# Kernel optimization log

Hardware: AMD Instinct MI355X
Metric: run time of the kernel (lower is better)

Reference implementation:

```python
import jax, jax.numpy as jnp
import numpy as np

H = 128      # hidden_channels
L = 4        # num_layers
B = 8192     # graphs per batch
NB, NJ, NF = 4 * B, 12 * B, 4 * B   # base/joint/foot node counts (4 bases, 12 joints, 4 feet per graph)
NET = 8      # number of edge types


def _edges(key, E, n_src, n_dst):
    k1, k2 = jax.random.split(key)
    return jnp.stack([jax.random.randint(k1, (E,), 0, n_src),
                      jax.random.randint(k2, (E,), 0, n_dst)]).astype(jnp.int32)


def setup_inputs() -> dict:
    key = jax.random.key(0)
    ks = jax.random.split(key, 24)
    s = 0.02
    return {
        "x_base": jax.random.normal(ks[0], (NB, 1800), jnp.float32),
        "x_joint": jax.random.normal(ks[1], (NJ, 300), jnp.float32),
        "x_foot": jax.random.normal(ks[2], (NF, 900), jnp.float32),
        "enc_W_base": jax.random.normal(ks[3], (H, 1800), jnp.float32) * s,
        "enc_b_base": jnp.zeros((H,), jnp.float32),
        "enc_W_joint": jax.random.normal(ks[4], (H, 300), jnp.float32) * s,
        "enc_b_joint": jnp.zeros((H,), jnp.float32),
        "enc_W_foot": jax.random.normal(ks[5], (H, 900), jnp.float32) * s,
        "enc_b_foot": jnp.zeros((H,), jnp.float32),
        "conv_Wrel": jax.random.normal(ks[6], (L, NET, H, H), jnp.float32) * s,
        "conv_Wroot": jax.random.normal(ks[7], (L, NET, H, H), jnp.float32) * s,
        "conv_brel": jnp.zeros((L, NET, H), jnp.float32),
        "bt_W1": jax.random.normal(ks[8], (H, H), jnp.float32) * s,
        "bt_b1": jnp.zeros((H,), jnp.float32),
        "bt_W2": jax.random.normal(ks[9], (H, H), jnp.float32) * s,
        "bt_b2": jnp.zeros((H,), jnp.float32),
        "dec_W": jax.random.normal(ks[10], (24, 4 * H), jnp.float32) * s,
        "dec_b": jnp.zeros((24,), jnp.float32),
        "coeff_lin": jnp.ones((12,), jnp.float32),   # base_coefficients for linear dims (ones when symmetry_mode=None)
        "coeff_ang": jnp.ones((12,), jnp.float32),
        "ei_bb_gt": _edges(ks[11], NB, NB, NB),
        "ei_bb_gs": _edges(ks[12], NB, NB, NB),
        "ei_bb_gr": _edges(ks[13], NB, NB, NB),
        "ei_bj": _edges(ks[14], NB, NB, NJ),
        "ei_jb": _edges(ks[15], NB, NJ, NB),
        "ei_jj": _edges(ks[16], 4 * NB, NJ, NJ),
        "ei_jf": _edges(ks[17], NF, NJ, NF),
        "ei_fj": _edges(ks[18], NF, NF, NJ),
    }


def _forward(floats, eidx):
    (x_base, x_joint, x_foot, enc_W_base, enc_b_base, enc_W_joint, enc_b_joint,
     enc_W_foot, enc_b_foot, conv_Wrel, conv_Wroot, conv_brel,
     bt_W1, bt_b1, bt_W2, bt_b2, dec_W, dec_b, coeff_lin, coeff_ang) = floats
    ei_bb_gt, ei_bb_gs, ei_bb_gr, ei_bj, ei_jb, ei_jj, ei_jf, ei_fj = eidx
    N = {"base": x_base.shape[0], "joint": x_joint.shape[0], "foot": x_foot.shape[0]}
    # HeteroDictLinear encoder + activation
    x = {"base": jax.nn.relu(x_base @ enc_W_base.T + enc_b_base),
         "joint": jax.nn.relu(x_joint @ enc_W_joint.T + enc_b_joint),
         "foot": jax.nn.relu(x_foot @ enc_W_foot.T + enc_b_foot)}
    # (src_type, dst_type, edge_index, mean_aggr?) -- 'gt'/'gs' use mean, all others add
    etypes = [("base", "base", ei_bb_gt, True), ("base", "base", ei_bb_gs, True),
              ("base", "base", ei_bb_gr, False), ("base", "joint", ei_bj, False),
              ("joint", "base", ei_jb, False), ("joint", "joint", ei_jj, False),
              ("joint", "foot", ei_jf, False), ("foot", "joint", ei_fj, False)]
    for l in range(L):
        new = {k: jnp.zeros_like(v) for k, v in x.items()}
        for t, (s_t, d_t, ei, is_mean) in enumerate(etypes):
            msg = x[s_t][ei[0]]                                        # gather [E, H]
            agg = jax.ops.segment_sum(msg, ei[1], num_segments=N[d_t])  # scatter-add [N_dst, H]
            if is_mean:
                deg = jax.ops.segment_sum(jnp.ones((ei.shape[1],), msg.dtype), ei[1], num_segments=N[d_t])
                agg = agg / jnp.maximum(deg, 1.0)[:, None]
            # PyG GraphConv: lin_rel(aggr(x_src)) + lin_root(x_dst); HeteroConv aggr='sum' over edge types
            new[d_t] = new[d_t] + agg @ conv_Wrel[l, t].T + conv_brel[l, t] + x[d_t] @ conv_Wroot[l, t].T
        base_new = jax.nn.relu(new["base"] @ bt_W1.T + bt_b1) @ bt_W2.T + bt_b2
        x = {"base": base_new + x["base"],
             "joint": jax.nn.relu(new["joint"]) + x["joint"],
             "foot": jax.nn.relu(new["foot"]) + x["foot"]}
    bs = N["base"] // 4
    out = x["base"].reshape(bs, 4 * H) @ dec_W.T + dec_b             # [bs, 24]
    # morphological_symmetry_decoder (coeffs are ones when symmetry_mode=None)
    xr = out.reshape(bs, 4, 6)
    x_lin = (xr[:, :, :3].reshape(bs, 12) * coeff_lin).reshape(bs, 4, 3)
    x_ang = (xr[:, :, 3:].reshape(bs, 12) * coeff_ang).reshape(bs, 4, 3)
    return jnp.concatenate([x_lin, x_ang], axis=-1).reshape(bs, 24)


def reference(x_base, x_joint, x_foot, enc_W_base, enc_b_base, enc_W_joint, enc_b_joint,
              enc_W_foot, enc_b_foot, conv_Wrel, conv_Wroot, conv_brel,
              bt_W1, bt_b1, bt_W2, bt_b2, dec_W, dec_b, coeff_lin, coeff_ang,
              ei_bb_gt, ei_bb_gs, ei_bb_gr, ei_bj, ei_jb, ei_jj, ei_jf, ei_fj):
    floats = (x_base, x_joint, x_foot, enc_W_base, enc_b_base, enc_W_joint, enc_b_joint,
              enc_W_foot, enc_b_foot, conv_Wrel, conv_Wroot, conv_brel,
              bt_W1, bt_b1, bt_W2, bt_b2, dec_W, dec_b, coeff_lin, coeff_ang)
    eidx = (ei_bb_gt, ei_bb_gs, ei_bb_gr, ei_bj, ei_jb, ei_jj, ei_jf, ei_fj)
    return _forward(floats, eidx)
```

## Files before the change

### kernel.cpp

```cpp
#include <hip/hip_runtime.h>

typedef __bf16 bf16;
typedef __attribute__((ext_vector_type(8))) __bf16 bf16x8;
typedef __attribute__((ext_vector_type(4))) float f32x4;
typedef __attribute__((ext_vector_type(4))) int   i32x4;

#define NBASE  32768
#define NJOINT 98304
#define NFOOT  32768
#define NSLOT  458752
#define NEDGE  360448
#define SCAN_BLOCKS 448

static __device__ __forceinline__ f32x4 mfma16(bf16x8 a, bf16x8 b, f32x4 c) {
  return __builtin_amdgcn_mfma_f32_16x16x32_bf16(a, b, c, 0, 0, 0);
}

static __device__ __forceinline__ void edge_decomp(int slot, int& ty, int& e) {
  if (slot < 131072)      { ty = slot >> 15; e = slot & 32767; }
  else if (slot < 163840) { ty = 4; e = slot - 131072; }
  else if (slot < 294912) { ty = 5; e = slot - 163840; }
  else if (slot < 327680) { ty = 6; e = slot - 294912; }
  else                    { ty = 7; e = slot - 327680; }
}
static __device__ __forceinline__ int type_off(int ty) {
  return ty==0?0: ty==1?32768: ty==2?65536: ty==3?98304:
         ty==4?196608: ty==5?229376: ty==6?327680: 360448;
}

struct EArgs { const int* e0; const int* e1; const int* e2; const int* e3;
               const int* e4; const int* e5; const int* e6; const int* e7; };
static __device__ __forceinline__ const int* esel(const EArgs& a, int ty) {
  const int* p = a.e0;
  if (ty==1) p=a.e1; if (ty==2) p=a.e2; if (ty==3) p=a.e3;
  if (ty==4) p=a.e4; if (ty==5) p=a.e5; if (ty==6) p=a.e6; if (ty==7) p=a.e7;
  return p;
}

__global__ __launch_bounds__(256) void prep_kernel(
    const float* __restrict__ Wrel, const float* __restrict__ Wroot,
    const float* __restrict__ brel, const float* __restrict__ bt1,
    const float* __restrict__ bt2,
    bf16* __restrict__ Wrel_b, bf16* __restrict__ Wroot_b,
    float* __restrict__ bias_s, bf16* __restrict__ bt1_b, bf16* __restrict__ bt2_b)
{
  int t = blockIdx.x * 256 + threadIdx.x;
  if (t < 4*8*16384) Wrel_b[t] = (bf16)Wrel[t];
  if (t < 4*3*16384) {
    int i = t & 16383; int ld = t >> 14; int l = ld / 3, dt = ld - l*3;
    const float* Wb = Wroot + l * 8 * 16384;
    float s;
    if (dt == 0)      s = Wb[0*16384+i] + Wb[1*16384+i] + Wb[2*16384+i] + Wb[4*16384+i];
    else if (dt == 1) s = Wb[3*16384+i] + Wb[5*16384+i] + Wb[7*16384+i];
    else              s = Wb[6*16384+i];
    Wroot_b[t] = (bf16)s;
  }
  if (t < 16384) { bt1_b[t] = (bf16)bt1[t]; bt2_b[t] = (bf16)bt2[t]; }
  if (t < 4*3*128) {
    int c = t & 127; int ld = t >> 7; int l = ld / 3, dt = ld - l*3;
    const float* B = brel + l * 8 * 128;
    float s;
    if (dt == 0)      s = B[0*128+c] + B[1*128+c] + B[2*128+c] + B[4*128+c];
    else if (dt == 1) s = B[3*128+c] + B[5*128+c] + B[7*128+c];
    else              s = B[6*128+c];
    bias_s[t] = s;
  }
}

__global__ __launch_bounds__(256) void zero_kernel(int* cnt) {
  cnt[blockIdx.x * 256 + threadIdx.x] = 0;
}

__global__ __launch_bounds__(256) void hist8_kernel(EArgs a, int* __restrict__ cnt) {
  int slot = blockIdx.x * 256 + threadIdx.x;
  int ty, e; edge_decomp(slot, ty, e);
  const int* ep = esel(a, ty);
  int ecnt = (ty == 5) ? 131072 : 32768;
  int dst = ep[ecnt + e];
  atomicAdd(&cnt[type_off(ty) + dst], 1);
}

__global__ __launch_bounds__(256) void scanA_kernel(const int* __restrict__ cnt, int* __restrict__ bsum) {
  __shared__ int red[256];
  int base = blockIdx.x * 1024 + threadIdx.x * 4;
  i32x4 v = *(const i32x4*)(cnt + base);
  red[threadIdx.x] = v[0] + v[1] + v[2] + v[3];
  __syncthreads();
  for (int d = 128; d > 0; d >>= 1) {
    if (threadIdx.x < d) red[threadIdx.x] += red[threadIdx.x + d];
    __syncthreads();
  }
  if (threadIdx.x == 0) bsum[blockIdx.x] = red[0];
}

__global__ __launch_bounds__(256) void scanB_kernel(const int* __restrict__ bsum, int* __restrict__ bscan) {
  __shared__ int s[SCAN_BLOCKS];
  int i0 = threadIdx.x, i1 = threadIdx.x + 256;
  bool h1 = (i1 < SCAN_BLOCKS);
  s[i0] = bsum[i0];
  if (h1) s[i1] = bsum[i1];
  __syncthreads();
  for (int d = 1; d < SCAN_BLOCKS; d <<= 1) {
    int v0 = 0, v1 = 0;
    if (i0 >= d) v0 = s[i0 - d];
    if (h1 && i1 >= d) v1 = s[i1 - d];
    __syncthreads();
    s[i0] += v0;
    if (h1) s[i1] += v1;
    __syncthreads();
  }
  bscan[i0] = i0 ? s[i0 - 1] : 0;
  if (h1) bscan[i1] = s[i1 - 1];
}

__global__ __launch_bounds__(256) void scanC_kernel(const int* __restrict__ cnt,
    const int* __restrict__ bscan, int* __restrict__ rowptr, int* __restrict__ cursor)
{
  __shared__ int toff[256];
  int base = blockIdx.x * 1024 + threadIdx.x * 4;
  i32x4 v = *(const i32x4*)(cnt + base);
  int tsum = v[0] + v[1] + v[2] + v[3];
  toff[threadIdx.x] = tsum;
  __syncthreads();
  for (int d = 1; d < 256; d <<= 1) {
    int t = 0;
    if (threadIdx.x >= d) t = toff[threadIdx.x - d];
    __syncthreads();
    toff[threadIdx.x] += t;
    __syncthreads();
  }
  int off = bscan[blockIdx.x] + toff[threadIdx.x] - tsum;
  i32x4 r;
  r[0] = off; r[1] = off + v[0]; r[2] = off + v[0] + v[1]; r[3] = off + v[0] + v[1] + v[2];
  *(i32x4*)(rowptr + base) = r;
  *(i32x4*)(cursor + base) = r;
  if (blockIdx.x == SCAN_BLOCKS - 1 && threadIdx.x == 255) rowptr[NSLOT] = NEDGE;
}

__global__ __launch_bounds__(256) void fill_kernel(EArgs a, int* __restrict__ cursor,
                                                   int* __restrict__ perm) {
  int slot = blockIdx.x * 256 + threadIdx.x;
  int ty, e; edge_decomp(slot, ty, e);
  const int* ep = esel(a, ty);
  int ecnt = (ty == 5) ? 131072 : 32768;
  int src = ep[e];
  int dst = ep[ecnt + e];
  int pos = atomicAdd(&cursor[type_off(ty) + dst], 1);
  perm[pos] = src;
}

template<int K>
__global__ __launch_bounds__(256) void enc_kernel(
    const float* __restrict__ X, const float* __restrict__ W,
    const float* __restrict__ bvec, bf16* __restrict__ out, float* __restrict__ out32)
{
  __shared__ bf16 Wl[4*128*8];
  const int tid = threadIdx.x;
  const int lane = tid & 63, wv = tid >> 6;
  const int r = lane & 15, g = lane >> 4;
  const long row = (long)blockIdx.x * 64 + wv * 16 + r;
  f32x4 acc[8] = {};
  for (int kc = 0; kc < K; kc += 32) {
    __syncthreads();
    for (int i = tid; i < 512; i += 256) {
      int q = i & 3, n = i >> 2;
      int k0 = kc + 8*q;
      f32x4 a = {}; f32x4 b2 = {};
      if (k0 < K)     a  = *(const f32x4*)(W + (long)n*K + k0);
      if (k0 + 4 < K) b2 = *(const f32x4*)(W + (long)n*K + k0 + 4);
      bf16x8 pk;
      #pragma unroll
      for (int j = 0; j < 4; j++) { pk[j] = (bf16)a[j]; pk[4+j] = (bf16)b2[j]; }
      *(bf16x8*)&Wl[(q*128 + (n ^ q)) * 8] = pk;
    }
    __syncthreads();
    int k0 = kc + 8*g;
    f32x4 a0 = {}, a1 = {};
    if (k0 < K)     a0 = *(const f32x4*)(X + row*K + k0);
    if (k0 + 4 < K) a1 = *(const f32x4*)(X + row*K + k0 + 4);
    bf16x8 af;
    #pragma unroll
    for (int j = 0; j < 4; j++) { af[j] = (bf16)a0[j]; af[4+j] = (bf16)a1[j]; }
    const bf16* bp = &Wl[(g*128 + (r ^ g)) * 8];
    #pragma unroll
    for (int c = 0; c < 8; c++) {
      bf16x8 bfr = *(const bf16x8*)(bp + c*128);
      acc[c] = mfma16(af, bfr, acc[c]);
    }
  }
  const long rb = (long)blockIdx.x * 64 + wv * 16 + 4 * g;
  #pragma unroll
  for (int c = 0; c < 8; c++) {
    int col = 16*c + r;
    float bb = bvec[col];
    #pragma unroll
    for (int j = 0; j < 4; j++) {
      float v = acc[c][j] + bb;
      v = v > 0.f ? v : 0.f;
      out[(rb + j)*128 + col] = (bf16)v;
      out32[(rb + j)*128 + col] = v;
    }
  }
}

struct GDesc { const void* A; const bf16* W; const float* bias; const float* res32;
               void* out; void* out2; int nblk; };
struct GArgs { GDesc d[8]; };

template<int EPI, bool AF32, int NDESC>
__global__ __launch_bounds__(256) void gemm128_kernel(GArgs a)
{
  __shared__ bf16 Wl[16*128*8];
  int b = blockIdx.x, di = 0;
  while (di + 1 < NDESC && b >= a.d[di].nblk) { b -= a.d[di].nblk; ++di; }
  const GDesc& D = a.d[di];
  const int tid = threadIdx.x;
  const int lane = tid & 63, wv = tid >> 6;
  const int r = lane & 15, g = lane >> 4;
  for (int i = tid; i < 2048; i += 256) {
    int q = i & 15, n = i >> 4;
    bf16x8 v = *(const bf16x8*)(D.W + n*128 + q*8);
    *(bf16x8*)&Wl[(q*128 + (n ^ (q & 7))) * 8] = v;
  }
  const long row = (long)b * 64 + wv * 16 + r;
  bf16x8 af[4];
  if constexpr (AF32) {
    const float* A = (const float*)D.A;
    #pragma unroll
    for (int kk = 0; kk < 4; kk++) {
      f32x4 a0 = *(const f32x4*)(A + row*128 + kk*32 + 8*g);
      f32x4 a1 = *(const f32x4*)(A + row*128 + kk*32 + 8*g + 4);
      #pragma unroll
      for (int j = 0; j < 4; j++) { af[kk][j] = (bf16)a0[j]; af[kk][4+j] = (bf16)a1[j]; }
    }
  } else {
    const bf16* A = (const bf16*)D.A;
    #pragma unroll
    for (int kk = 0; kk < 4; kk++)
      af[kk] = *(const bf16x8*)(A + row*128 + kk*32 + 8*g);
  }
  __syncthreads();
  f32x4 acc[8] = {};
  #pragma unroll
  for (int kk = 0; kk < 4; kk++) {
    int q = kk*4 + g;
    const bf16* bp = &Wl[(q*128 + (r ^ (q & 7))) * 8];
    #pragma unroll
    for (int c = 0; c < 8; c++) {
      bf16x8 bfr = *(const bf16x8*)(bp + c*128);
      acc[c] = mfma16(af[kk], bfr, acc[c]);
    }
  }
  const long rb = (long)b * 64 + wv * 16 + 4 * g;
  #pragma unroll
  for (int c = 0; c < 8; c++) {
    int col = 16*c + r;
    #pragma unroll
    for (int j = 0; j < 4; j++) {
      float v = acc[c][j];
      long oidx = (rb + j)*128 + col;
      if constexpr (EPI == 0) {
        ((float*)D.out)[oidx] = v + D.bias[col];
      } else if constexpr (EPI == 1) {
        ((bf16*)D.out)[oidx] = (bf16)v;
      } else if constexpr (EPI == 2) {
        v += D.bias[col];
        v = v > 0.f ? v : 0.f;
        ((bf16*)D.out)[oidx] = (bf16)v;
      } else {
        v += D.bias[col] + D.res32[oidx];
        ((bf16*)D.out)[oidx] = (bf16)v;
        ((float*)D.out2)[oidx] = v;
      }
    }
  }
}

struct AArgs { const bf16* y[4]; const float* root; float* o32; bf16* o16; };

template<int KIND>
__global__ __launch_bounds__(256) void agg_kernel(AArgs a,
    const int* __restrict__ rowptr, const int* __restrict__ perm)
{
  constexpr int NT = (KIND==0) ? 4 : ((KIND==1) ? 3 : 1);
  constexpr int OFFS[3][4] = {{0, 32768, 65536, 196608},
                              {98304, 229376, 360448, 0},
                              {327680, 0, 0, 0}};
  const int tid = threadIdx.x;
  const int lane = tid & 63, wv = tid >> 6;
  const int l8 = lane & 15, g = lane >> 4;
  const int node = blockIdx.x * 16 + wv * 4 + g;
  const long co = (long)node * 128 + l8 * 8;
  f32x4 a0 = *(const f32x4*)(a.root + co);
  f32x4 a1 = *(const f32x4*)(a.root + co + 4);
  #pragma unroll
  for (int ti = 0; ti < NT; ++ti) {
    const int slot = OFFS[KIND][ti] + node;
    int rp0 = rowptr[slot], rp1 = rowptr[slot + 1];
    float sc = 1.0f;
    if (KIND == 0 && ti < 2) {
      int d = rp1 - rp0;
      sc = d > 0 ? 1.0f / (float)d : 1.0f;
    }
    const bf16* yb = a.y[ti];
    for (int e = rp0; e < rp1; ++e) {
      int src = perm[e];
      bf16x8 v = *(const bf16x8*)(yb + (long)src * 128 + l8 * 8);
      #pragma unroll
      for (int j = 0; j < 4; j++) {
        a0[j] += (float)v[j]   * sc;
        a1[j] += (float)v[4+j] * sc;
      }
    }
  }
  if constexpr (KIND == 0) {
    *(f32x4*)(a.o32 + co)     = a0;
    *(f32x4*)(a.o32 + co + 4) = a1;
  } else {
    f32x4 x0 = *(const f32x4*)(a.o32 + co);
    f32x4 x1 = *(const f32x4*)(a.o32 + co + 4);
    bf16x8 ov;
    #pragma unroll
    for (int j = 0; j < 4; j++) {
      float v0 = (a0[j] > 0.f ? a0[j] : 0.f) + x0[j];
      float v1 = (a1[j] > 0.f ? a1[j] : 0.f) + x1[j];
      x0[j] = v0; x1[j] = v1;
      ov[j] = (bf16)v0; ov[4+j] = (bf16)v1;
    }
    *(f32x4*)(a.o32 + co)     = x0;
    *(f32x4*)(a.o32 + co + 4) = x1;
    *(bf16x8*)(a.o16 + co)    = ov;
  }
}

__global__ __launch_bounds__(256) void dec_kernel(const float* __restrict__ xb32,
    const float* __restrict__ W, const float* __restrict__ bvec,
    const float* __restrict__ clin, const float* __restrict__ cang,
    float* __restrict__ out)
{
  __shared__ float Wl[24*512];
  const int tid = threadIdx.x;
  for (int i = tid; i < 3072; i += 256)
    *(f32x4*)&Wl[i*4] = *(const f32x4*)(W + i*4);
  __syncthreads();
  const long row = (long)blockIdx.x * 256 + tid;
  float acc[24] = {};
  for (int k0 = 0; k0 < 512; k0 += 4) {
    f32x4 xv = *(const f32x4*)(xb32 + row*512 + k0);
    #pragma unroll
    for (int n = 0; n < 24; n++) {
      const float* wr = &Wl[n*512 + k0];
      float s = acc[n];
      #pragma unroll
      for (int j = 0; j < 4; j++) s += xv[j] * wr[j];
      acc[n] = s;
    }
  }
  #pragma unroll
  for (int n = 0; n < 24; n++) {
    int gq = n / 6, c = n - gq*6;
    float coef = (c < 3) ? clin[gq*3 + c] : cang[gq*3 + c - 3];
    out[row*24 + n] = (acc[n] + bvec[n]) * coef;
  }
}

extern "C" void kernel_launch(void* const* d_in, const int* in_sizes, int n_in,
                              void* d_out, int out_size, void* d_ws, size_t ws_size,
                              hipStream_t stream)
{
  const float* x_base  = (const float*)d_in[0];
  const float* x_joint = (const float*)d_in[1];
  const float* x_foot  = (const float*)d_in[2];
  const float* eWb  = (const float*)d_in[3];
  const float* ebb  = (const float*)d_in[4];
  const float* eWj  = (const float*)d_in[5];
  const float* ebj  = (const float*)d_in[6];
  const float* eWf  = (const float*)d_in[7];
  const float* ebf  = (const float*)d_in[8];
  const float* Wrel  = (const float*)d_in[9];
  const float* Wroot = (const float*)d_in[10];
  const float* brel  = (const float*)d_in[11];
  const float* btW1  = (const float*)d_in[12];
  const float* btb1  = (const float*)d_in[13];
  const float* btW2  = (const float*)d_in[14];
  const float* btb2  = (const float*)d_in[15];
  const float* decW  = (const float*)d_in[16];
  const float* decb  = (const float*)d_in[17];
  const float* clin  = (const float*)d_in[18];
  const float* cang  = (const float*)d_in[19];
  const int* ei[8];
  for (int t = 0; t < 8; t++) ei[t] = (const int*)d_in[20 + t];

  char* p = (char*)d_ws;
  auto alloc = [&](size_t bytes) { char* r = p; p += (bytes + 255) & ~(size_t)255; return r; };
  bf16*  xb    = (bf16*) alloc((size_t)NBASE  * 128 * 2);
  bf16*  xj    = (bf16*) alloc((size_t)NJOINT * 128 * 2);
  bf16*  xf    = (bf16*) alloc((size_t)NFOOT  * 128 * 2);
  float* xb32  = (float*)alloc((size_t)NBASE  * 128 * 4);
  float* xj32  = (float*)alloc((size_t)NJOINT * 128 * 4);
  float* xf32  = (float*)alloc((size_t)NFOOT  * 128 * 4);
  float* new_b = (float*)alloc((size_t)NBASE  * 128 * 4);
  float* new_j = (float*)alloc((size_t)NJOINT * 128 * 4);
  float* new_f = (float*)alloc((size_t)NFOOT  * 128 * 4);
  const size_t ySrc[8] = {NBASE, NBASE, NBASE, NBASE, NJOINT, NJOINT, NJOINT, NFOOT};
  bf16* y[8];
  for (int t = 0; t < 8; t++) y[t] = (bf16*)alloc(ySrc[t] * 128 * 2);
  bf16*  hbt     = (bf16*) alloc((size_t)NBASE * 128 * 2);
  bf16*  Wrel_b  = (bf16*) alloc(4*8*16384*2);
  bf16*  Wroot_b = (bf16*) alloc(4*3*16384*2);
  bf16*  bt1_b   = (bf16*) alloc(16384*2);
  bf16*  bt2_b   = (bf16*) alloc(16384*2);
  float* bias_s  = (float*)alloc(4*3*128*4);
  int*   cnt     = (int*)  alloc((size_t)NSLOT*4);
  int*   rowptr  = (int*)  alloc((size_t)(NSLOT+1)*4);
  int*   cursor  = (int*)  alloc((size_t)NSLOT*4);
  int*   perm    = (int*)  alloc((size_t)NEDGE*4);
  int*   bsum    = (int*)  alloc((size_t)SCAN_BLOCKS*4);
  int*   bscan   = (int*)  alloc((size_t)SCAN_BLOCKS*4);
  (void)ws_size; (void)in_sizes; (void)n_in; (void)out_size;

  EArgs ea = { ei[0], ei[1], ei[2], ei[3], ei[4], ei[5], ei[6], ei[7] };

  prep_kernel<<<2048, 256, 0, stream>>>(Wrel, Wroot, brel, btW1, btW2,
                                        Wrel_b, Wroot_b, bias_s, bt1_b, bt2_b);
  zero_kernel<<<NSLOT/256, 256, 0, stream>>>(cnt);
  hist8_kernel<<<NEDGE/256, 256, 0, stream>>>(ea, cnt);
  scanA_kernel<<<SCAN_BLOCKS, 256, 0, stream>>>(cnt, bsum);
  scanB_kernel<<<1, 256, 0, stream>>>(bsum, bscan);
  scanC_kernel<<<SCAN_BLOCKS, 256, 0, stream>>>(cnt, bscan, rowptr, cursor);
  fill_kernel<<<NEDGE/256, 256, 0, stream>>>(ea, cursor, perm);

  enc_kernel<1800><<<512,  256, 0, stream>>>(x_base,  eWb, ebb, xb, xb32);
  enc_kernel<300> <<<1536, 256, 0, stream>>>(x_joint, eWj, ebj, xj, xj32);
  enc_kernel<900> <<<512,  256, 0, stream>>>(x_foot,  eWf, ebf, xf, xf32);

  const bf16* xsrc[8] = {xb, xb, xb, xb, xj, xj, xj, xf};
  const int nblkSrc[8] = {512, 512, 512, 512, 1536, 1536, 1536, 512};

  for (int l = 0; l < 4; l++) {
    GArgs ra = {};
    for (int t = 0; t < 8; t++)
      ra.d[t] = GDesc{ xsrc[t], Wrel_b + (l*8 + t)*16384, nullptr, nullptr, y[t], nullptr, nblkSrc[t] };
    gemm128_kernel<1, false, 8><<<7168, 256, 0, stream>>>(ra);

    GArgs ro = {};
    ro.d[0] = GDesc{ xb, Wroot_b + (l*3 + 0)*16384, bias_s + (l*3 + 0)*128, nullptr, new_b, nullptr, 512 };
    ro.d[1] = GDesc{ xj, Wroot_b + (l*3 + 1)*16384, bias_s + (l*3 + 1)*128, nullptr, new_j, nullptr, 1536 };
    ro.d[2] = GDesc{ xf, Wroot_b + (l*3 + 2)*16384, bias_s + (l*3 + 2)*128, nullptr, new_f, nullptr, 512 };
    gemm128_kernel<0, false, 3><<<2560, 256, 0, stream>>>(ro);

    AArgs ab = { { y[0], y[1], y[2], y[4] }, new_b, new_b, nullptr };
    agg_kernel<0><<<NBASE/16, 256, 0, stream>>>(ab, rowptr, perm);
    AArgs aj = { { y[3], y[5], y[7], nullptr }, new_j, xj32, xj };
    agg_kernel<1><<<NJOINT/16, 256, 0, stream>>>(aj, rowptr, perm);
    AArgs af = { { y[6], nullptr, nullptr, nullptr }, new_f, xf32, xf };
    agg_kernel<2><<<NFOOT/16, 256, 0, stream>>>(af, rowptr, perm);

    GArgs b1 = {};
    b1.d[0] = GDesc{ new_b, bt1_b, btb1, nullptr, hbt, nullptr, 512 };
    gemm128_kernel<2, true, 1><<<512, 256, 0, stream>>>(b1);

    GArgs b2a = {};
    b2a.d[0] = GDesc{ hbt, bt2_b, btb2, xb32, xb, xb32, 512 };
    gemm128_kernel<3, false, 1><<<512, 256, 0, stream>>>(b2a);
  }

  dec_kernel<<<32, 256, 0, stream>>>(xb32, decW, decb, clin, cang, (float*)d_out);
}
```

Baseline: 1.603 ms.

## Pre-pack encoder weights to bf16, double-buffer encoder K-loop, merge rel/root GEMM launches

Encoder weights are converted to padded bf16 once in the prep kernel. The encoder now walks K in 128-wide stages with double-buffered shared memory and register prefetch of the next stage's W and X, which removes the per-32-K fp32 weight conversion and halves the barriers. The per-layer relation and root GEMM launches are merged into one 11-descriptor launch with a runtime epilogue selector, saving a launch per layer. The cost is more shared memory and registers per block, plus extra K padding work.

Measured after the change: 1.479 ms. -7.8%, faster.

```diff
diff --git a/kernel.cpp b/kernel.cpp
--- a/kernel.cpp
+++ b/kernel.cpp
@@ -41,8 +41,11 @@
     const float* __restrict__ Wrel, const float* __restrict__ Wroot,
     const float* __restrict__ brel, const float* __restrict__ bt1,
     const float* __restrict__ bt2,
+    const float* __restrict__ eWb, const float* __restrict__ eWj,
+    const float* __restrict__ eWf,
     bf16* __restrict__ Wrel_b, bf16* __restrict__ Wroot_b,
-    float* __restrict__ bias_s, bf16* __restrict__ bt1_b, bf16* __restrict__ bt2_b)
+    float* __restrict__ bias_s, bf16* __restrict__ bt1_b, bf16* __restrict__ bt2_b,
+    bf16* __restrict__ eWb_p, bf16* __restrict__ eWj_p, bf16* __restrict__ eWf_p)
 {
   int t = blockIdx.x * 256 + threadIdx.x;
   if (t < 4*8*16384) Wrel_b[t] = (bf16)Wrel[t];
@@ -65,6 +68,12 @@
     else              s = B[6*128+c];
     bias_s[t] = s;
   }
+  if (t < 128*1920) { int n = t / 1920, k = t - n*1920;
+    eWb_p[t] = (bf16)(k < 1800 ? eWb[n*1800 + k] : 0.f); }
+  if (t < 128*384)  { int n = t / 384, k = t - n*384;
+    eWj_p[t] = (bf16)(k < 300 ? eWj[n*300 + k] : 0.f); }
+  if (t < 128*1024) { int n = t >> 10, k = t & 1023;
+    eWf_p[t] = (bf16)(k < 900 ? eWf[n*900 + k] : 0.f); }
 }
 
 __global__ __launch_bounds__(256) void zero_kernel(int* cnt) {
@@ -149,63 +158,99 @@
   perm[pos] = src;
 }
 
-template<int K>
-__global__ __launch_bounds__(256) void enc_kernel(
-    const float* __restrict__ X, const float* __restrict__ W,
+template<int K, int KP>
+__global__ __launch_bounds__(256) void enc2_kernel(
+    const float* __restrict__ X, const bf16* __restrict__ Wp,
     const float* __restrict__ bvec, bf16* __restrict__ out, float* __restrict__ out32)
 {
-  __shared__ bf16 Wl[4*128*8];
+  constexpr int S = KP / 128;
+  __shared__ bf16 Wl[2][2048 * 8];
   const int tid = threadIdx.x;
   const int lane = tid & 63, wv = tid >> 6;
   const int r = lane & 15, g = lane >> 4;
   const long row = (long)blockIdx.x * 64 + wv * 16 + r;
+  const float* xrow = X + row * (long)K;
+
+  bf16x8 wreg[8];
+  f32x4 xa[8], xb[8];
+
+  auto WLOAD = [&](int s) {
+    const int kc = s * 128;
+    #pragma unroll
+    for (int j = 0; j < 8; j++) {
+      int i = tid + j * 256;
+      int n = i >> 4, q = i & 15;
+      wreg[j] = *(const bf16x8*)(Wp + n * KP + kc + 8 * q);
+    }
+  };
+  auto WWRITE = [&](int buf) {
+    #pragma unroll
+    for (int j = 0; j < 8; j++) {
+      int i = tid + j * 256;
+      int n = i >> 4, q = i & 15;
+      *(bf16x8*)&Wl[buf][(q * 128 + (n ^ (q & 7))) * 8] = wreg[j];
+    }
+  };
+  auto XLOAD = [&](int s, f32x4* xr) {
+    const int kc = s * 128;
+    #pragma unroll
+    for (int c = 0; c < 4; c++) {
+      int k0 = kc + 32 * c + 8 * g;
+      xr[2*c]   = (k0     < K) ? *(const f32x4*)(xrow + k0)     : f32x4{0.f,0.f,0.f,0.f};
+      xr[2*c+1] = (k0 + 4 < K) ? *(const f32x4*)(xrow + k0 + 4) : f32x4{0.f,0.f,0.f,0.f};
+    }
+  };
+
+  WLOAD(0); XLOAD(0, xa); WWRITE(0);
   f32x4 acc[8] = {};
-  for (int kc = 0; kc < K; kc += 32) {
+
+  #pragma unroll 2
+  for (int s = 0; s < S; s++) {
     __syncthreads();
-    for (int i = tid; i < 512; i += 256) {
-      int q = i & 3, n = i >> 2;
-      int k0 = kc + 8*q;
-      f32x4 a = {}; f32x4 b2 = {};
-      if (k0 < K)     a  = *(const f32x4*)(W + (long)n*K + k0);
-      if (k0 + 4 < K) b2 = *(const f32x4*)(W + (long)n*K + k0 + 4);
-      bf16x8 pk;
+    if (s + 1 < S) { WLOAD(s + 1); XLOAD(s + 1, xb); WWRITE((s + 1) & 1); }
+    bf16x8 af[4];
+    #pragma unroll
+    for (int c = 0; c < 4; c++) {
       #pragma unroll
-      for (int j = 0; j < 4; j++) { pk[j] = (bf16)a[j]; pk[4+j] = (bf16)b2[j]; }
-      *(bf16x8*)&Wl[(q*128 + (n ^ q)) * 8] = pk;
-    }
-    __syncthreads();
-    int k0 = kc + 8*g;
-    f32x4 a0 = {}, a1 = {};
-    if (k0 < K)     a0 = *(const f32x4*)(X + row*K + k0);
-    if (k0 + 4 < K) a1 = *(const f32x4*)(X + row*K + k0 + 4);
-    bf16x8 af;
-    #pragma unroll
-    for (int j = 0; j < 4; j++) { af[j] = (bf16)a0[j]; af[4+j] = (bf16)a1[j]; }
-    const bf16* bp = &Wl[(g*128 + (r ^ g)) * 8];
-    #pragma unroll
-    for (int c = 0; c < 8; c++) {
-      bf16x8 bfr = *(const bf16x8*)(bp + c*128);
-      acc[c] = mfma16(af, bfr, acc[c]);
-    }
-  }
+      for (int j = 0; j < 4; j++) {
+        af[c][j]     = (bf16)xa[2*c][j];
+        af[c][4 + j] = (bf16)xa[2*c+1][j];
+      }
+    }
+    #pragma unroll
+    for (int c = 0; c < 4; c++) {
+      const int q = 4 * c + g;
+      const bf16* bp = &Wl[s & 1][(q * 128 + (r ^ (q & 7))) * 8];
+      #pragma unroll
+      for (int cc = 0; cc < 8; cc++) {
+        bf16x8 bfr = *(const bf16x8*)(bp + cc * 128);
+        acc[cc] = mfma16(af[c], bfr, acc[cc]);
+      }
+    }
+    if (s + 1 < S) {
+      #pragma unroll
+      for (int k = 0; k < 8; k++) xa[k] = xb[k];
+    }
+  }
+
   const long rb = (long)blockIdx.x * 64 + wv * 16 + 4 * g;
   #pragma unroll
   for (int c = 0; c < 8; c++) {
-    int col = 16*c + r;
+    int col = 16 * c + r;
     float bb = bvec[col];
     #pragma unroll
     for (int j = 0; j < 4; j++) {
       float v = acc[c][j] + bb;
       v = v > 0.f ? v : 0.f;
-      out[(rb + j)*128 + col] = (bf16)v;
-      out32[(rb + j)*128 + col] = v;
+      out[(rb + j) * 128 + col] = (bf16)v;
+      out32[(rb + j) * 128 + col] = v;
     }
   }
 }
 
 struct GDesc { const void* A; const bf16* W; const float* bias; const float* res32;
-               void* out; void* out2; int nblk; };
-struct GArgs { GDesc d[8]; };
+               void* out; void* out2; int nblk; int epi; };
+struct GArgs { GDesc d[11]; };
 
 template<int EPI, bool AF32, int NDESC>
 __global__ __launch_bounds__(256) void gemm128_kernel(GArgs a)
@@ -259,7 +304,10 @@
     for (int j = 0; j < 4; j++) {
       float v = acc[c][j];
       long oidx = (rb + j)*128 + col;
-      if constexpr (EPI == 0) {
+      if constexpr (EPI == -1) {
+        if (D.epi == 0) ((float*)D.out)[oidx] = v + D.bias[col];
+        else            ((bf16*)D.out)[oidx] = (bf16)v;
+      } else if constexpr (EPI == 0) {
         ((float*)D.out)[oidx] = v + D.bias[col];
       } else if constexpr (EPI == 1) {
         ((bf16*)D.out)[oidx] = (bf16)v;
@@ -411,6 +459,9 @@
   bf16*  bt1_b   = (bf16*) alloc(16384*2);
   bf16*  bt2_b   = (bf16*) alloc(16384*2);
   float* bias_s  = (float*)alloc(4*3*128*4);
+  bf16*  eWb_p   = (bf16*) alloc((size_t)128*1920*2);
+  bf16*  eWj_p   = (bf16*) alloc((size_t)128*384*2);
+  bf16*  eWf_p   = (bf16*) alloc((size_t)128*1024*2);
   int*   cnt     = (int*)  alloc((size_t)NSLOT*4);
   int*   rowptr  = (int*)  alloc((size_t)(NSLOT+1)*4);
   int*   cursor  = (int*)  alloc((size_t)NSLOT*4);
@@ -422,7 +473,9 @@
   EArgs ea = { ei[0], ei[1], ei[2], ei[3], ei[4], ei[5], ei[6], ei[7] };
 
   prep_kernel<<<2048, 256, 0, stream>>>(Wrel, Wroot, brel, btW1, btW2,
-                                        Wrel_b, Wroot_b, bias_s, bt1_b, bt2_b);
+                                        eWb, eWj, eWf,
+                                        Wrel_b, Wroot_b, bias_s, bt1_b, bt2_b,
+                                        eWb_p, eWj_p, eWf_p);
   zero_kernel<<<NSLOT/256, 256, 0, stream>>>(cnt);
   hist8_kernel<<<NEDGE/256, 256, 0, stream>>>(ea, cnt);
   scanA_kernel<<<SCAN_BLOCKS, 256, 0, stream>>>(cnt, bsum);
@@ -430,9 +483,9 @@
   scanC_kernel<<<SCAN_BLOCKS, 256, 0, stream>>>(cnt, bscan, rowptr, cursor);
   fill_kernel<<<NEDGE/256, 256, 0, stream>>>(ea, cursor, perm);
 
-  enc_kernel<1800><<<512,  256, 0, stream>>>(x_base,  eWb, ebb, xb, xb32);
-  enc_kernel<300> <<<1536, 256, 0, stream>>>(x_joint, eWj, ebj, xj, xj32);
-  enc_kernel<900> <<<512,  256, 0, stream>>>(x_foot,  eWf, ebf, xf, xf32);
+  enc2_kernel<1800,1920><<<512,  256, 0, stream>>>(x_base,  eWb_p, ebb, xb, xb32);
+  enc2_kernel<300, 384> <<<1536, 256, 0, stream>>>(x_joint, eWj_p, ebj, xj, xj32);
+  enc2_kernel<900, 1024><<<512,  256, 0, stream>>>(x_foot,  eWf_p, ebf, xf, xf32);
 
   const bf16* xsrc[8] = {xb, xb, xb, xb, xj, xj, xj, xf};
   const int nblkSrc[8] = {512, 512, 512, 512, 1536, 1536, 1536, 512};
@@ -440,14 +493,15 @@
   for (int l = 0; l < 4; l++) {
     GArgs ra = {};
     for (int t = 0; t < 8; t++)
-      ra.d[t] = GDesc{ xsrc[t], Wrel_b + (l*8 + t)*16384, nullptr, nullptr, y[t], nullptr, nblkSrc[t] };
-    gemm128_kernel<1, false, 8><<<7168, 256, 0, stream>>>(ra);
-
-    GArgs ro = {};
-    ro.d[0] = GDesc{ xb, Wroot_b + (l*3 + 0)*16384, bias_s + (l*3 + 0)*128, nullptr, new_b, nullptr, 512 };
-    ro.d[1] = GDesc{ xj, Wroot_b + (l*3 + 1)*16384, bias_s + (l*3 + 1)*128, nullptr, new_j, nullptr, 1536 };
-    ro.d[2] = GDesc{ xf, Wroot_b + (l*3 + 2)*16384, bias_s + (l*3 + 2)*128, nullptr, new_f, nullptr, 512 };
-    gemm128_kernel<0, false, 3><<<2560, 256, 0, stream>>>(ro);
+      ra.d[t] = GDesc{ xsrc[t], Wrel_b + (l*8 + t)*16384, nullptr, nullptr,
+                       y[t], nullptr, nblkSrc[t], 1 };
+    ra.d[8]  = GDesc{ xb, Wroot_b + (l*3 + 0)*16384, bias_s + (l*3 + 0)*128, nullptr,
+                      new_b, nullptr, 512, 0 };
+    ra.d[9]  = GDesc{ xj, Wroot_b + (l*3 + 1)*16384, bias_s + (l*3 + 1)*128, nullptr,
+                      new_j, nullptr, 1536, 0 };
+    ra.d[10] = GDesc{ xf, Wroot_b + (l*3 + 2)*16384, bias_s + (l*3 + 2)*128, nullptr,
+                      new_f, nullptr, 512, 0 };
+    gemm128_kernel<-1, false, 11><<<9728, 256, 0, stream>>>(ra);
 
     AArgs ab = { { y[0], y[1], y[2], y[4] }, new_b, new_b, nullptr };
     agg_kernel<0><<<NBASE/16, 256, 0, stream>>>(ab, rowptr, perm);
@@ -457,11 +511,11 @@
     agg_kernel<2><<<NFOOT/16, 256, 0, stream>>>(af, rowptr, perm);
 
     GArgs b1 = {};
-    b1.d[0] = GDesc{ new_b, bt1_b, btb1, nullptr, hbt, nullptr, 512 };
+    b1.d[0] = GDesc{ new_b, bt1_b, btb1, nullptr, hbt, nullptr, 512, 2 };
     gemm128_kernel<2, true, 1><<<512, 256, 0, stream>>>(b1);
 
     GArgs b2a = {};
-    b2a.d[0] = GDesc{ hbt, bt2_b, btb2, xb32, xb, xb32, 512 };
+    b2a.d[0] = GDesc{ hbt, bt2_b, btb2, xb32, xb, xb32, 512, 3 };
     gemm128_kernel<3, false, 1><<<512, 256, 0, stream>>>(b2a);
   }
 
```
